# Optimization experiments

Measured on AMD Instinct MI355X. Metric: run time of the kernel, lower is better.

The kernel has to match this reference:

```python
import jax, jax.numpy as jnp
import numpy as np

VOCAB, E, H = 32000, 256, 256
B, T = 64, 2048


def setup_inputs() -> dict:
    key = jax.random.key(0)
    ks = jax.random.split(key, 6)
    X = jax.random.randint(ks[0], (B, T), 0, VOCAB)
    emb = jax.random.normal(ks[1], (VOCAB, E), dtype=jnp.float32)
    W_qrnn = jax.random.normal(ks[2], (E, 3 * H), dtype=jnp.float32) / np.sqrt(E)
    b_qrnn = jnp.zeros((3 * H,), dtype=jnp.float32)
    c0 = jax.random.normal(ks[3], (B, H), dtype=jnp.float32)
    W_out = jax.random.normal(ks[4], (H, 1), dtype=jnp.float32) / np.sqrt(H)
    b_out = jnp.zeros((1,), dtype=jnp.float32)
    return {"X": X, "emb": emb, "W_qrnn": W_qrnn, "b_qrnn": b_qrnn,
            "c0": c0, "W_out": W_out, "b_out": b_out}


def reference(X, emb, W_qrnn, b_qrnn, c0, W_out, b_out):
    # Embedding lookup: [B,T] -> [B,T,E]; permute to seq-major [T,B,E]
    x = jnp.transpose(emb[X], (1, 0, 2))
    # QRNN window=1 gate projection: all timesteps in one GEMM, [T,B,3H]
    g = jnp.einsum('tbe,ef->tbf', x, W_qrnn) + b_qrnn
    z, f, o = jnp.split(g, 3, axis=-1)
    z = jnp.tanh(z)
    f = jax.nn.sigmoid(f)
    o = jax.nn.sigmoid(o)

    # fo-pooling recurrence: c_t = f_t * c_{t-1} + (1 - f_t) * z_t
    def step(c, zf):
        z_t, f_t = zf
        c = f_t * c + (1.0 - f_t) * z_t
        return c, c

    _, cs = jax.lax.scan(step, c0, (z, f))  # cs: [T,B,H]
    h = o * cs                              # h_t = o_t * c_t
    hn = h[-1]                              # last timestep, [B,H]
    return hn @ W_out + b_out               # [B,1]
```

## Files before the change

kernel.cpp:

```cpp
#include <hip/hip_runtime.h>
#include <hip/hip_bf16.h>
#include <math.h>

#define EDIM 256
#define HDIM 256
#define BDIM 64
#define TDIM 2048
#define NC   64
#define TC   32
#define CPB  4

typedef __attribute__((ext_vector_type(8)))  short  short8;
typedef __attribute__((ext_vector_type(4)))  float  floatx4;
typedef __attribute__((ext_vector_type(4)))  unsigned int uintx4;

__device__ __forceinline__ unsigned short f2bf(float f) {
    unsigned int u = __float_as_uint(f);
    u += 0x7FFFu + ((u >> 16) & 1u);
    return (unsigned short)(u >> 16);
}
__device__ __forceinline__ unsigned int pk2(float a, float b) {
    return (unsigned int)f2bf(a) | ((unsigned int)f2bf(b) << 16);
}
__device__ __forceinline__ float sigm(float x) {
    return __builtin_amdgcn_rcpf(1.f + __expf(-x));
}
__device__ __forceinline__ float tanh_fast(float x) {
    return fmaf(-2.f, __builtin_amdgcn_rcpf(1.f + __expf(2.f * x)), 1.f);
}

__global__ __launch_bounds__(256) void qrnn_pack(
    const float* __restrict__ Wq, const float* __restrict__ emb,
    unsigned short* __restrict__ Wp, unsigned short* __restrict__ ebf,
    int mode)
{
    const int bx = blockIdx.x;
    if (bx < 256) {
        const int nt = (bx >> 3) & 7;
        const int hg = bx >> 6;
        const int ks = bx & 7;
        const int t = threadIdx.x;
        const int lane = t >> 2, pj = t & 3;
        const int col = lane & 15, q = lane >> 4;
        const int h = hg * 64 + (nt & 3) * 16 + col;
        const int c = (nt < 4) ? h : (HDIM + h);
        const int k = ks * 32 + q * 8 + pj * 2;
        unsigned int v = pk2(Wq[k * (3 * HDIM) + c], Wq[(k + 1) * (3 * HDIM) + c]);
        *(unsigned int*)(Wp + (size_t)bx * 512 + lane * 8 + pj * 2) = v;
    } else if (mode == 1) {
        size_t i = ((size_t)(bx - 256) * 256 + threadIdx.x) * 8;
        floatx4 a = *(const floatx4*)(emb + i);
        floatx4 b = *(const floatx4*)(emb + i + 4);
        uintx4 o = {pk2(a.x, a.y), pk2(a.z, a.w), pk2(b.x, b.y), pk2(b.z, b.w)};
        *(uintx4*)(ebf + i) = o;
    }
}

template<int MODE>
__global__ __launch_bounds__(512, 2) void qrnn_mfma(
    const int* __restrict__ X, const float* __restrict__ emb,
    const unsigned short* __restrict__ ebf, const unsigned short* __restrict__ Wp,
    const float* __restrict__ bq, float* __restrict__ wsA, float* __restrict__ wsB)
{
    __shared__ __align__(16) short Bsh[32768];

    const int tid = threadIdx.x;
    const int cg = blockIdx.x, bg = blockIdx.y, hg = blockIdx.z;
    const int lane = tid & 63, w = tid >> 6;
    const int col = lane & 15, q = lane >> 4;

    const unsigned short* wpb = Wp + (size_t)hg * 32768;
#pragma unroll
    for (int i = 0; i < 8; ++i) {
        const int ch = w * 8 + i;
        __builtin_amdgcn_global_load_lds(
            (const __attribute__((address_space(1))) unsigned int*)(wpb + ch * 512 + lane * 8),
            (__attribute__((address_space(3))) unsigned int*)(Bsh + ch * 512),
            16, 0, 0);
    }

    const int b0 = bg * 8 + w;
    int xid[CPB][2];
#pragma unroll
    for (int c = 0; c < CPB; ++c)
#pragma unroll
        for (int mt = 0; mt < 2; ++mt)
            xid[c][mt] = X[b0 * TDIM + (cg * CPB + c) * TC + mt * 16 + col];

    const int hbase = hg * 64;
    float bz[4], bff[4];
#pragma unroll
    for (int nt = 0; nt < 4; ++nt) {
        bz[nt]  = bq[hbase + nt * 16 + col];
        bff[nt] = bq[HDIM + hbase + nt * 16 + col];
    }

    floatx4 acc[2][8];
#pragma unroll
    for (int mt = 0; mt < 2; ++mt)
#pragma unroll
        for (int nt = 0; nt < 8; ++nt) acc[mt][nt] = (floatx4){0.f, 0.f, 0.f, 0.f};

    __syncthreads();

#pragma unroll
    for (int c = 0; c < CPB; ++c) {
        short8 abuf[8][2];
#pragma unroll
        for (int ks = 0; ks < 8; ++ks)
#pragma unroll
            for (int mt = 0; mt < 2; ++mt) {
                if constexpr (MODE == 1) {
                    abuf[ks][mt] = *(const short8*)(ebf + (size_t)xid[c][mt] * EDIM + q * 8 + ks * 32);
                } else {
                    const float* ap = emb + (size_t)xid[c][mt] * EDIM + q * 8 + ks * 32;
                    floatx4 f0 = *(const floatx4*)ap;
                    floatx4 f1 = *(const floatx4*)(ap + 4);
                    uintx4 p = {pk2(f0.x, f0.y), pk2(f0.z, f0.w),
                                pk2(f1.x, f1.y), pk2(f1.z, f1.w)};
                    abuf[ks][mt] = *(short8*)&p;
                }
            }

#pragma unroll
        for (int ks = 0; ks < 8; ++ks) {
            short8 bf[8];
#pragma unroll
            for (int nt = 0; nt < 8; ++nt)
                bf[nt] = *(const short8*)(Bsh + (nt * 8 + ks) * 512 + lane * 8);
#pragma unroll
            for (int nt = 0; nt < 8; ++nt)
#pragma unroll
                for (int mt = 0; mt < 2; ++mt)
                    acc[mt][nt] = __builtin_amdgcn_mfma_f32_16x16x32_bf16(abuf[ks][mt], bf[nt], acc[mt][nt], 0, 0, 0);
        }

        const int cc = cg * CPB + c;
        float Af[4], Bf[4];
#pragma unroll
        for (int nt = 0; nt < 4; ++nt) {
            float Aseg[2], Bseg[2];
#pragma unroll
            for (int mt = 0; mt < 2; ++mt) {
                float Ac = 1.f, Bc = 0.f;
#pragma unroll
                for (int j = 0; j < 4; ++j) {
                    float z = tanh_fast(acc[mt][nt][j] + bz[nt]);
                    float f = sigm(acc[mt][nt + 4][j] + bff[nt]);
                    Ac = f * Ac;
                    Bc = fmaf(f, Bc, (1.f - f) * z);
                }
                Aseg[mt] = Ac; Bseg[mt] = Bc;
            }
#pragma unroll
            for (int st = 0; st < 2; ++st) {
                const int msk = 16 << st;
                const bool self_earlier = ((q >> st) & 1) == 0;
#pragma unroll
                for (int mt = 0; mt < 2; ++mt) {
                    float Ap = __shfl_xor(Aseg[mt], msk, 64);
                    float Bp = __shfl_xor(Bseg[mt], msk, 64);
                    Bseg[mt] = self_earlier ? fmaf(Ap, Bseg[mt], Bp)
                                            : fmaf(Aseg[mt], Bp, Bseg[mt]);
                    Aseg[mt] = Aseg[mt] * Ap;
                }
            }
            Af[nt] = Aseg[0] * Aseg[1];
            Bf[nt] = fmaf(Aseg[1], Bseg[0], Bseg[1]);
        }

        float As = (q == 0) ? Af[0] : (q == 1) ? Af[1] : (q == 2) ? Af[2] : Af[3];
        float Bs = (q == 0) ? Bf[0] : (q == 1) ? Bf[1] : (q == 2) ? Bf[2] : Bf[3];

        const size_t r0 = ((size_t)cc * BDIM + b0) * HDIM + hbase + lane;
        wsA[r0] = As;
        wsB[r0] = Bs;

#pragma unroll
        for (int mt = 0; mt < 2; ++mt)
#pragma unroll
            for (int nt = 0; nt < 8; ++nt) acc[mt][nt] = (floatx4){0.f, 0.f, 0.f, 0.f};
    }
}

__global__ __launch_bounds__(256) void qrnn_combine(
    const float* __restrict__ wsA, const float* __restrict__ wsB,
    const float* __restrict__ c0, const int* __restrict__ X,
    const float* __restrict__ emb, const float* __restrict__ Wq,
    const float* __restrict__ bq, const float* __restrict__ Wout,
    const float* __restrict__ bout, float* __restrict__ out)
{
    const int b = blockIdx.x;
    const int h = threadIdx.x;

    float c = c0[b * HDIM + h];
    for (int c8 = 0; c8 < NC; c8 += 8) {
        float a[8], bb[8];
#pragma unroll
        for (int i = 0; i < 8; ++i) {
            size_t base = ((size_t)(c8 + i) * BDIM + b) * HDIM + h;
            a[i]  = wsA[base];
            bb[i] = wsB[base];
        }
#pragma unroll
        for (int i = 0; i < 8; ++i) c = fmaf(a[i], c, bb[i]);
    }

    __shared__ float xs[EDIM];
    int idx = X[b * TDIM + (TDIM - 1)];
    xs[h] = emb[(size_t)idx * EDIM + h];
    __syncthreads();

    float acc = 0.f;
#pragma unroll 16
    for (int e = 0; e < EDIM; ++e)
        acc = fmaf(xs[e], Wq[e * (3 * HDIM) + 2 * HDIM + h], acc);

    float o  = 1.f / (1.f + expf(-(acc + bq[2 * HDIM + h])));
    float hn = o * c;

    __shared__ float red[HDIM];
    red[h] = hn * Wout[h];
    __syncthreads();
    for (int s = HDIM / 2; s > 0; s >>= 1) {
        if (h < s) red[h] += red[h + s];
        __syncthreads();
    }
    if (h == 0) out[b] = red[0] + bout[0];
}

extern "C" void kernel_launch(void* const* d_in, const int* in_sizes, int n_in,
                              void* d_out, int out_size, void* d_ws, size_t ws_size,
                              hipStream_t stream) {
    const int*   X    = (const int*)d_in[0];
    const float* emb  = (const float*)d_in[1];
    const float* Wq   = (const float*)d_in[2];
    const float* bq   = (const float*)d_in[3];
    const float* c0   = (const float*)d_in[4];
    const float* Wout = (const float*)d_in[5];
    const float* bout = (const float*)d_in[6];
    float* out = (float*)d_out;

    float* wsA = (float*)d_ws;
    float* wsB = wsA + (size_t)NC * BDIM * HDIM;
    unsigned short* Wp  = (unsigned short*)(wsB + (size_t)NC * BDIM * HDIM);
    unsigned short* ebf = Wp + (size_t)256 * 512;

    const size_t wsAB = (size_t)2 * NC * BDIM * HDIM * 4;
    const size_t wpsz = (size_t)256 * 512 * 2;
    const size_t need1 = wsAB + wpsz + (size_t)32000 * EDIM * 2;
    const int mode = (ws_size >= need1) ? 1 : 0;

    const int gather_blocks = (mode == 1) ? (32000 * EDIM / 8) / 256 : 0;
    qrnn_pack<<<256 + gather_blocks, 256, 0, stream>>>(Wq, emb, Wp, ebf, mode);

    dim3 g(NC / CPB, BDIM / 8, HDIM / 64);
    if (mode == 1) qrnn_mfma<1><<<g, 512, 0, stream>>>(X, emb, ebf, Wp, bq, wsA, wsB);
    else           qrnn_mfma<0><<<g, 512, 0, stream>>>(X, emb, ebf, Wp, bq, wsA, wsB);

    qrnn_combine<<<BDIM, 256, 0, stream>>>(wsA, wsB, c0, X, emb, Wq, bq, Wout, bout, out);
}
```

Before: 144.8 us.

## Reuse gathered embedding tile across all hidden groups instead of re-gathering per group

Each block now gathers its embedding A-tile once and loops over the four hidden-column groups, restaging the weight slice into LDS per group with barriers. Before, each hidden group was a separate block that gathered the same rows again, and each block walked four time chunks with a single weight slice. This quarters the embedding gather traffic but serializes the weight staging against compute, since the next slice load is issued only after the current MFMAs finish. It also adds extra syncthreads per iteration, and the grid changes shape to 64x8x1 (still 512 blocks).

Measured after the change: 159.3 us. 10.1% more time.

```diff
diff --git a/kernel.cpp b/kernel.cpp
--- a/kernel.cpp
+++ b/kernel.cpp
@@ -8,7 +8,6 @@
 #define TDIM 2048
 #define NC   64
 #define TC   32
-#define CPB  4
 
 typedef __attribute__((ext_vector_type(8)))  short  short8;
 typedef __attribute__((ext_vector_type(4)))  float  floatx4;
@@ -65,62 +64,63 @@
     __shared__ __align__(16) short Bsh[32768];
 
     const int tid = threadIdx.x;
-    const int cg = blockIdx.x, bg = blockIdx.y, hg = blockIdx.z;
+    const int cg = blockIdx.x, bg = blockIdx.y;
     const int lane = tid & 63, w = tid >> 6;
     const int col = lane & 15, q = lane >> 4;
 
-    const unsigned short* wpb = Wp + (size_t)hg * 32768;
-#pragma unroll
-    for (int i = 0; i < 8; ++i) {
-        const int ch = w * 8 + i;
-        __builtin_amdgcn_global_load_lds(
-            (const __attribute__((address_space(1))) unsigned int*)(wpb + ch * 512 + lane * 8),
-            (__attribute__((address_space(3))) unsigned int*)(Bsh + ch * 512),
-            16, 0, 0);
-    }
-
     const int b0 = bg * 8 + w;
-    int xid[CPB][2];
-#pragma unroll
-    for (int c = 0; c < CPB; ++c)
+    int xid[2];
+#pragma unroll
+    for (int mt = 0; mt < 2; ++mt)
+        xid[mt] = X[b0 * TDIM + cg * TC + mt * 16 + col];
+
+    short8 abuf[8][2];
+#pragma unroll
+    for (int ks = 0; ks < 8; ++ks)
+#pragma unroll
+        for (int mt = 0; mt < 2; ++mt) {
+            if constexpr (MODE == 1) {
+                abuf[ks][mt] = *(const short8*)(ebf + (size_t)xid[mt] * EDIM + q * 8 + ks * 32);
+            } else {
+                const float* ap = emb + (size_t)xid[mt] * EDIM + q * 8 + ks * 32;
+                floatx4 f0 = *(const floatx4*)ap;
+                floatx4 f1 = *(const floatx4*)(ap + 4);
+                uintx4 p = {pk2(f0.x, f0.y), pk2(f0.z, f0.w),
+                            pk2(f1.x, f1.y), pk2(f1.z, f1.w)};
+                abuf[ks][mt] = *(short8*)&p;
+            }
+        }
+    __builtin_amdgcn_sched_barrier(0);
+
+    auto stage = [&](int hg) {
+        const unsigned short* wpb = Wp + (size_t)hg * 32768;
+#pragma unroll
+        for (int i = 0; i < 8; ++i) {
+            const int ch = w * 8 + i;
+            __builtin_amdgcn_global_load_lds(
+                (const __attribute__((address_space(1))) unsigned int*)(wpb + ch * 512 + lane * 8),
+                (__attribute__((address_space(3))) unsigned int*)(Bsh + ch * 512),
+                16, 0, 0);
+        }
+    };
+    stage(0);
+    __syncthreads();
+
+#pragma unroll 1
+    for (int hg = 0; hg < 4; ++hg) {
+        const int hbase = hg * 64;
+        float bz[4], bff[4];
+#pragma unroll
+        for (int nt = 0; nt < 4; ++nt) {
+            bz[nt]  = bq[hbase + nt * 16 + col];
+            bff[nt] = bq[HDIM + hbase + nt * 16 + col];
+        }
+
+        floatx4 acc[2][8];
 #pragma unroll
         for (int mt = 0; mt < 2; ++mt)
-            xid[c][mt] = X[b0 * TDIM + (cg * CPB + c) * TC + mt * 16 + col];
-
-    const int hbase = hg * 64;
-    float bz[4], bff[4];
-#pragma unroll
-    for (int nt = 0; nt < 4; ++nt) {
-        bz[nt]  = bq[hbase + nt * 16 + col];
-        bff[nt] = bq[HDIM + hbase + nt * 16 + col];
-    }
-
-    floatx4 acc[2][8];
-#pragma unroll
-    for (int mt = 0; mt < 2; ++mt)
-#pragma unroll
-        for (int nt = 0; nt < 8; ++nt) acc[mt][nt] = (floatx4){0.f, 0.f, 0.f, 0.f};
-
-    __syncthreads();
-
-#pragma unroll
-    for (int c = 0; c < CPB; ++c) {
-        short8 abuf[8][2];
-#pragma unroll
-        for (int ks = 0; ks < 8; ++ks)
-#pragma unroll
-            for (int mt = 0; mt < 2; ++mt) {
-                if constexpr (MODE == 1) {
-                    abuf[ks][mt] = *(const short8*)(ebf + (size_t)xid[c][mt] * EDIM + q * 8 + ks * 32);
-                } else {
-                    const float* ap = emb + (size_t)xid[c][mt] * EDIM + q * 8 + ks * 32;
-                    floatx4 f0 = *(const floatx4*)ap;
-                    floatx4 f1 = *(const floatx4*)(ap + 4);
-                    uintx4 p = {pk2(f0.x, f0.y), pk2(f0.z, f0.w),
-                                pk2(f1.x, f1.y), pk2(f1.z, f1.w)};
-                    abuf[ks][mt] = *(short8*)&p;
-                }
-            }
+#pragma unroll
+            for (int nt = 0; nt < 8; ++nt) acc[mt][nt] = (floatx4){0.f, 0.f, 0.f, 0.f};
 
 #pragma unroll
         for (int ks = 0; ks < 8; ++ks) {
@@ -135,7 +135,9 @@
                     acc[mt][nt] = __builtin_amdgcn_mfma_f32_16x16x32_bf16(abuf[ks][mt], bf[nt], acc[mt][nt], 0, 0, 0);
         }
 
-        const int cc = cg * CPB + c;
+        __syncthreads();
+        if (hg < 3) stage(hg + 1);
+
         float Af[4], Bf[4];
 #pragma unroll
         for (int nt = 0; nt < 4; ++nt) {
@@ -172,14 +174,11 @@
         float As = (q == 0) ? Af[0] : (q == 1) ? Af[1] : (q == 2) ? Af[2] : Af[3];
         float Bs = (q == 0) ? Bf[0] : (q == 1) ? Bf[1] : (q == 2) ? Bf[2] : Bf[3];
 
-        const size_t r0 = ((size_t)cc * BDIM + b0) * HDIM + hbase + lane;
+        const size_t r0 = ((size_t)cg * BDIM + b0) * HDIM + hbase + lane;
         wsA[r0] = As;
         wsB[r0] = Bs;
 
-#pragma unroll
-        for (int mt = 0; mt < 2; ++mt)
-#pragma unroll
-            for (int nt = 0; nt < 8; ++nt) acc[mt][nt] = (floatx4){0.f, 0.f, 0.f, 0.f};
+        __syncthreads();
     }
 }
 
@@ -254,7 +253,7 @@
     const int gather_blocks = (mode == 1) ? (32000 * EDIM / 8) / 256 : 0;
     qrnn_pack<<<256 + gather_blocks, 256, 0, stream>>>(Wq, emb, Wp, ebf, mode);
 
-    dim3 g(NC / CPB, BDIM / 8, HDIM / 64);
+    dim3 g(NC, BDIM / 8, 1);
     if (mode == 1) qrnn_mfma<1><<<g, 512, 0, stream>>>(X, emb, ebf, Wp, bq, wsA, wsB);
     else           qrnn_mfma<0><<<g, 512, 0, stream>>>(X, emb, ebf, Wp, bq, wsA, wsB);
 
```
